# Kernel tuning notes

Measured on AMD Instinct MI355X. Metric: run time of the kernel, lower is better.

The kernel has to match this reference:

```python
import jax, jax.numpy as jnp
import numpy as np

EMBED_DIM = 2048
HEAD_DIM = 128
BLOCK = 2048
BATCH = 8


def setup_inputs() -> dict:
    key = jax.random.key(0)
    kx, kq, kk, kv = jax.random.split(key, 4)
    x = jax.random.normal(kx, (BATCH, BLOCK, EMBED_DIM), dtype=jnp.float32)
    # torch nn.Linear(embed_dim, head_dim, bias=False) weight shape: [head_dim, embed_dim]
    s = 1.0 / np.sqrt(EMBED_DIM)
    Wq = jax.random.uniform(kq, (HEAD_DIM, EMBED_DIM), jnp.float32, -s, s)
    Wk = jax.random.uniform(kk, (HEAD_DIM, EMBED_DIM), jnp.float32, -s, s)
    Wv = jax.random.uniform(kv, (HEAD_DIM, EMBED_DIM), jnp.float32, -s, s)
    return {"x": x, "Wq": Wq, "Wk": Wk, "Wv": Wv}


def reference(x, Wq, Wk, Wv):
    B, T, C = x.shape
    # projections: y = x @ W.T
    q = jnp.einsum('btc,hc->bth', x, Wq)   # [B,T,H]
    k = jnp.einsum('btc,hc->bth', x, Wk)
    v = jnp.einsum('btc,hc->bth', x, Wv)
    # NOTE: original scales by embed_dim**0.5, not head_dim**0.5
    scale = 1.0 / jnp.sqrt(jnp.float32(C))
    logits = jnp.einsum('bth,bsh->bts', q, k) * scale  # [B,T,T]
    # causal mask (is_decoder=True)
    causal = jnp.tril(jnp.ones((T, T), dtype=bool))
    logits = jnp.where(causal, logits, -jnp.inf)
    weights = jax.nn.softmax(logits, axis=-1)
    attention = jnp.einsum('bts,bsh->bth', weights, v)  # [B,T,H]
    return attention
```

## Files before the change

kernel.cpp:

```cpp
#include <hip/hip_runtime.h>
#include <hip/hip_bf16.h>
#include <stdint.h>

constexpr int B    = 8;
constexpr int T    = 2048;
constexpr int EMB  = 2048;
constexpr int HD   = 128;
constexpr int M    = B * T;
constexpr int NW   = 3 * HD;

typedef __attribute__((ext_vector_type(8))) short short8;
typedef __attribute__((ext_vector_type(4))) float f32x4;

__device__ inline unsigned short f2bf(float f) {
    union { float f; unsigned int u; } v; v.f = f;
    unsigned int x = v.u;
    unsigned int r = (x + 0x7FFFu + ((x >> 16) & 1u)) >> 16;
    return (unsigned short)r;
}

__device__ inline unsigned int cvt_pk_bf16(float a, float b) {
    unsigned int r;
    asm volatile("v_cvt_pk_bf16_f32 %0, %1, %2" : "=v"(r) : "v"(a), "v"(b));
    return r;
}

__global__ __launch_bounds__(256) void conv_w(
    const float* __restrict__ Wq, const float* __restrict__ Wk, const float* __restrict__ Wv,
    unsigned short* __restrict__ Wb)
{
    int base = (blockIdx.x * 256 + threadIdx.x) * 8;
    int row = base >> 11, col = base & 2047;
    const float* src;
    if (row < 128)      src = Wq + (size_t)row * EMB + col;
    else if (row < 256) src = Wk + (size_t)(row - 128) * EMB + col;
    else                src = Wv + (size_t)(row - 256) * EMB + col;
    float4 a = *(const float4*)src;
    float4 b = *(const float4*)(src + 4);
    short8 sv;
    sv[0] = f2bf(a.x); sv[1] = f2bf(a.y); sv[2] = f2bf(a.z); sv[3] = f2bf(a.w);
    sv[4] = f2bf(b.x); sv[5] = f2bf(b.y); sv[6] = f2bf(b.z); sv[7] = f2bf(b.w);
    *(short8*)(Wb + base) = sv;
}

constexpr int PBM = 64;
constexpr int PBK = 64;
constexpr int PNT = EMB / PBK;

__global__ __launch_bounds__(512) void qkv_proj(
    const float* __restrict__ x, const unsigned short* __restrict__ Wb,
    unsigned short* __restrict__ Qb, unsigned short* __restrict__ Kb,
    unsigned short* __restrict__ VtG)
{
    __shared__ unsigned short Asm[2][PBM * PBK];
    __shared__ unsigned short Bsm[2][NW * PBK];

    const int m0   = blockIdx.x * PBM;
    const int tid  = threadIdx.x;
    const int lane = tid & 63;
    const int w    = tid >> 6;
    const int wr   = w >> 2;
    const int wc   = w & 3;
    const int lo   = lane & 15;
    const int hi   = lane >> 4;

    const int ar = tid >> 3;
    const int as = tid & 7;
    const float* asrc = x + (size_t)(m0 + ar) * EMB + as * 8;

    f32x4 acc[2][6];
#pragma unroll
    for (int i = 0; i < 2; ++i)
#pragma unroll
        for (int j = 0; j < 6; ++j) acc[i][j] = (f32x4)0.0f;

    float4 a0, a1;
    auto issueA = [&](int k0) {
        a0 = *(const float4*)(asrc + k0);
        a1 = *(const float4*)(asrc + k0 + 4);
    };
    auto writeA = [&](int buf) {
        uint4 p;
        p.x = cvt_pk_bf16(a0.x, a0.y);
        p.y = cvt_pk_bf16(a0.z, a0.w);
        p.z = cvt_pk_bf16(a1.x, a1.y);
        p.w = cvt_pk_bf16(a1.z, a1.w);
        int ps = as ^ (ar & 7);
        *(uint4*)&Asm[buf][ar * PBK + ps * 8] = p;
    };
    auto stageB = [&](int k0, int buf) {
#pragma unroll
        for (int it = 0; it < 6; ++it) {
            int c = it * 512 + tid;
            int row = c >> 3;
            int lseg = (c & 7) ^ (row & 7);
            __builtin_amdgcn_global_load_lds(
                (const __attribute__((address_space(1))) unsigned int*)
                    (Wb + (size_t)row * EMB + k0 + lseg * 8),
                (__attribute__((address_space(3))) unsigned int*)
                    ((char*)&Bsm[buf][0] + (it * 512 + w * 64) * 16),
                16, 0, 0);
        }
    };
    auto compute = [&](int buf) {
#pragma unroll
        for (int kk = 0; kk < 2; ++kk) {
            short8 af[2], bf[6];
#pragma unroll
            for (int i = 0; i < 2; ++i) {
                int R = wr * 32 + i * 16 + lo;
                int pseg = (kk * 4 + hi) ^ (R & 7);
                af[i] = *(const short8*)&Asm[buf][R * PBK + pseg * 8];
            }
#pragma unroll
            for (int j = 0; j < 6; ++j) {
                int n = wc * 96 + j * 16 + lo;
                int pseg = (kk * 4 + hi) ^ (n & 7);
                bf[j] = *(const short8*)&Bsm[buf][n * PBK + pseg * 8];
            }
#pragma unroll
            for (int i = 0; i < 2; ++i)
#pragma unroll
                for (int j = 0; j < 6; ++j)
                    acc[i][j] = __builtin_amdgcn_mfma_f32_16x16x32_bf16(af[i], bf[j], acc[i][j], 0, 0, 0);
        }
    };

    issueA(0);
    stageB(0, 0);
    writeA(0);
    asm volatile("s_waitcnt vmcnt(0) lgkmcnt(0)" ::: "memory");
    __builtin_amdgcn_s_barrier();

    for (int t = 0; t < PNT; ++t) {
        const int buf = t & 1;
        if (t + 1 < PNT) {
            issueA((t + 1) * PBK);
            stageB((t + 1) * PBK, buf ^ 1);
        }
        compute(buf);
        if (t + 1 < PNT) {
            writeA(buf ^ 1);
            asm volatile("s_waitcnt vmcnt(0) lgkmcnt(0)" ::: "memory");
            __builtin_amdgcn_s_barrier();
        }
    }

    const int b = m0 >> 11;
#pragma unroll
    for (int i = 0; i < 2; ++i) {
        int mrow0 = m0 + wr * 32 + i * 16 + hi * 4;
#pragma unroll
        for (int j = 0; j < 6; ++j) {
            int cw = wc * 6 + j;
            int colbase = cw * 16 + lo;
            if (cw < 8) {
#pragma unroll
                for (int r = 0; r < 4; ++r)
                    Qb[(size_t)(mrow0 + r) * HD + colbase] = f2bf(acc[i][j][r]);
            } else if (cw < 16) {
#pragma unroll
                for (int r = 0; r < 4; ++r)
                    Kb[(size_t)(mrow0 + r) * HD + (colbase - 128)] = f2bf(acc[i][j][r]);
            } else {
                int h = colbase - 256;
                int tloc = mrow0 - b * T;
                ushort4 pv;
                pv.x = f2bf(acc[i][j][0]); pv.y = f2bf(acc[i][j][1]);
                pv.z = f2bf(acc[i][j][2]); pv.w = f2bf(acc[i][j][3]);
                *(ushort4*)(VtG + ((size_t)(b * HD + h)) * T + tloc) = pv;
            }
        }
    }
}

constexpr int QB = 64;
constexpr int KB = 64;
constexpr int STILES = 8;

__global__ __launch_bounds__(256) void attn_fwd(
    const unsigned short* __restrict__ Qb,
    const unsigned short* __restrict__ Kb,
    const unsigned short* __restrict__ VtG,
    float* __restrict__ out,
    float* __restrict__ part_o, float* __restrict__ part_ml,
    int use_split)
{
    const int b  = blockIdx.y;
    int bx = blockIdx.x;
    int qt, s, nsplit;
    if (use_split) {
        if (bx < 8)       { qt = bx;               s = 0; }
        else if (bx < 24) { qt = 8  + (bx - 8) / 2;  s = (bx - 8) & 1; }
        else if (bx < 48) { qt = 16 + (bx - 24) / 3; s = (bx - 24) % 3; }
        else              { qt = 24 + (bx - 48) / 4; s = (bx - 48) & 3; }
        nsplit = qt / 8 + 1;
    } else {
        qt = bx; s = 0; nsplit = 1;
    }
    const int q0 = qt * QB;
    int t0 = s * STILES;
    int t1 = t0 + STILES; if (t1 > qt + 1) t1 = qt + 1;

    const int tid  = threadIdx.x;
    const int lane = tid & 63;
    const int w    = tid >> 6;
    const int lo   = lane & 15;
    const int hi   = lane >> 4;

    __shared__ unsigned short Ks[KB][HD + 8];
    __shared__ unsigned short Vt[HD][KB + 16];
    __shared__ unsigned short Ps[QB][KB + 8];

    short8 qf[4];
    {
        int row = q0 + w * 16 + lo;
        const unsigned short* qp = Qb + ((size_t)b * T + row) * HD + hi * 8;
#pragma unroll
        for (int ks = 0; ks < 4; ++ks) qf[ks] = *(const short8*)(qp + ks * 32);
    }

    float mrow[4], lrow[4];
    f32x4 o[8];
#pragma unroll
    for (int r = 0; r < 4; ++r) { mrow[r] = -1e30f; lrow[r] = 0.0f; }
#pragma unroll
    for (int n = 0; n < 8; ++n) o[n] = (f32x4)0.0f;

    const float scale2 = 0.022097086912079608f * 1.4426950408889634f;
    const int qrow_base = q0 + w * 16 + hi * 4;

    for (int t = t0; t < t1; ++t) {
        const int kv0 = t * KB;
#pragma unroll
        for (int it = 0; it < 4; ++it) {
            int c = tid + it * 256;
            int row = c >> 4, c8 = (c & 15) * 8;
            *(short8*)&Ks[row][c8] =
                *(const short8*)(Kb + ((size_t)b * T + kv0 + row) * HD + c8);
        }
#pragma unroll
        for (int it = 0; it < 4; ++it) {
            int c = tid + it * 256;
            int row = c >> 3, c8 = (c & 7) * 8;
            *(short8*)&Vt[row][c8] =
                *(const short8*)(VtG + (size_t)(b * HD + row) * T + kv0 + c8);
        }
        __syncthreads();

        f32x4 sa[4];
#pragma unroll
        for (int j = 0; j < 4; ++j) sa[j] = (f32x4)0.0f;
#pragma unroll
        for (int ks = 0; ks < 4; ++ks) {
#pragma unroll
            for (int j = 0; j < 4; ++j) {
                short8 bf = *(const short8*)&Ks[j * 16 + lo][ks * 32 + hi * 8];
                sa[j] = __builtin_amdgcn_mfma_f32_16x16x32_bf16(qf[ks], bf, sa[j], 0, 0, 0);
            }
        }

        const bool diag = (t == qt);
        float alpha[4];
#pragma unroll
        for (int r = 0; r < 4; ++r) {
            const int qrow = qrow_base + r;
            float rm = -1e30f;
#pragma unroll
            for (int j = 0; j < 4; ++j) {
                float v = sa[j][r] * scale2;
                if (diag) {
                    int kv = kv0 + j * 16 + lo;
                    v = (kv <= qrow) ? v : -1e30f;
                }
                sa[j][r] = v;
                rm = fmaxf(rm, v);
            }
            rm = fmaxf(rm, __shfl_xor(rm, 1));
            rm = fmaxf(rm, __shfl_xor(rm, 2));
            rm = fmaxf(rm, __shfl_xor(rm, 4));
            rm = fmaxf(rm, __shfl_xor(rm, 8));
            float mn = fmaxf(mrow[r], rm);
            alpha[r] = exp2f(mrow[r] - mn);
            mrow[r] = mn;
            float ls = 0.0f;
#pragma unroll
            for (int j = 0; j < 4; ++j) {
                float p = exp2f(sa[j][r] - mn);
                sa[j][r] = p;
                ls += p;
            }
            ls += __shfl_xor(ls, 1);
            ls += __shfl_xor(ls, 2);
            ls += __shfl_xor(ls, 4);
            ls += __shfl_xor(ls, 8);
            lrow[r] = lrow[r] * alpha[r] + ls;
        }
#pragma unroll
        for (int n = 0; n < 8; ++n)
#pragma unroll
            for (int r = 0; r < 4; ++r) o[n][r] *= alpha[r];

#pragma unroll
        for (int r = 0; r < 4; ++r)
#pragma unroll
            for (int j = 0; j < 4; ++j)
                Ps[w * 16 + hi * 4 + r][j * 16 + lo] = f2bf(sa[j][r]);
        __syncthreads();

#pragma unroll
        for (int ks = 0; ks < 2; ++ks) {
            short8 af = *(const short8*)&Ps[w * 16 + lo][ks * 32 + hi * 8];
#pragma unroll
            for (int n = 0; n < 8; ++n) {
                short8 bv = *(const short8*)&Vt[n * 16 + lo][ks * 32 + hi * 8];
                o[n] = __builtin_amdgcn_mfma_f32_16x16x32_bf16(af, bv, o[n], 0, 0, 0);
            }
        }
        __syncthreads();
    }

    if (nsplit == 1) {
#pragma unroll
        for (int n = 0; n < 8; ++n) {
            int h = n * 16 + lo;
#pragma unroll
            for (int r = 0; r < 4; ++r) {
                int row = qrow_base + r;
                out[((size_t)b * T + row) * HD + h] = o[n][r] / lrow[r];
            }
        }
    } else {
        const size_t slot = (size_t)(b * 32 + qt) * 4 + s;
        float* po = part_o + slot * (QB * HD);
#pragma unroll
        for (int n = 0; n < 8; ++n) {
            int h = n * 16 + lo;
#pragma unroll
            for (int r = 0; r < 4; ++r)
                po[(w * 16 + hi * 4 + r) * HD + h] = o[n][r];
        }
        if (lo == 0) {
            float* pm = part_ml + slot * (QB * 2);
#pragma unroll
            for (int r = 0; r < 4; ++r) {
                pm[(w * 16 + hi * 4 + r) * 2 + 0] = mrow[r];
                pm[(w * 16 + hi * 4 + r) * 2 + 1] = lrow[r];
            }
        }
    }
}

__global__ __launch_bounds__(256) void attn_combine(
    const float* __restrict__ part_o, const float* __restrict__ part_ml,
    float* __restrict__ out)
{
    const int qt = 8 + blockIdx.x;
    const int b  = blockIdx.y;
    const int ns = qt / 8 + 1;
    const int tid = threadIdx.x;
    const int row = tid >> 2;
    const int c0  = (tid & 3) * 32;
    const size_t slot0 = (size_t)(b * 32 + qt) * 4;

    float mi[4], li[4];
    float m = -1e30f;
#pragma unroll 4
    for (int i = 0; i < ns; ++i) {
        mi[i] = part_ml[(slot0 + i) * (QB * 2) + row * 2 + 0];
        li[i] = part_ml[(slot0 + i) * (QB * 2) + row * 2 + 1];
        m = fmaxf(m, mi[i]);
    }
    float L = 0.0f, f[4];
#pragma unroll 4
    for (int i = 0; i < ns; ++i) {
        f[i] = exp2f(mi[i] - m);
        L += li[i] * f[i];
    }
    const float inv = 1.0f / L;

    float4 acc[8];
#pragma unroll
    for (int k = 0; k < 8; ++k) acc[k] = make_float4(0.f, 0.f, 0.f, 0.f);
#pragma unroll 4
    for (int i = 0; i < ns; ++i) {
        const float4* src = (const float4*)(part_o + (slot0 + i) * (QB * HD) + row * HD + c0);
#pragma unroll
        for (int k = 0; k < 8; ++k) {
            float4 v = src[k];
            acc[k].x += f[i] * v.x; acc[k].y += f[i] * v.y;
            acc[k].z += f[i] * v.z; acc[k].w += f[i] * v.w;
        }
    }
    float4* dst = (float4*)(out + ((size_t)b * T + qt * QB + row) * HD + c0);
#pragma unroll
    for (int k = 0; k < 8; ++k) {
        float4 v = acc[k];
        dst[k] = make_float4(v.x * inv, v.y * inv, v.z * inv, v.w * inv);
    }
}

extern "C" void kernel_launch(void* const* d_in, const int* in_sizes, int n_in,
                              void* d_out, int out_size, void* d_ws, size_t ws_size,
                              hipStream_t stream)
{
    const float* x  = (const float*)d_in[0];
    const float* Wq = (const float*)d_in[1];
    const float* Wk = (const float*)d_in[2];
    const float* Wv = (const float*)d_in[3];
    float* out = (float*)d_out;

    const size_t off_Wb = 0;
    const size_t off_Q  = off_Wb + (size_t)NW * EMB * 2;
    const size_t off_K  = off_Q  + (size_t)M * HD * 2;
    const size_t off_V  = off_K  + (size_t)M * HD * 2;
    const size_t off_po = off_V  + (size_t)M * HD * 2;
    const size_t off_ml = off_po + (size_t)1024 * QB * HD * 4;
    const size_t total  = off_ml + (size_t)1024 * QB * 2 * 4;

    char* ws = (char*)d_ws;
    unsigned short* Wb  = (unsigned short*)(ws + off_Wb);
    unsigned short* Qb  = (unsigned short*)(ws + off_Q);
    unsigned short* Kb  = (unsigned short*)(ws + off_K);
    unsigned short* VtG = (unsigned short*)(ws + off_V);
    float* part_o  = (float*)(ws + off_po);
    float* part_ml = (float*)(ws + off_ml);

    const int use_split = (ws_size >= total) ? 1 : 0;

    conv_w<<<dim3((NW * EMB) / (256 * 8)), 256, 0, stream>>>(Wq, Wk, Wv, Wb);
    qkv_proj<<<dim3(M / PBM), 512, 0, stream>>>(x, Wb, Qb, Kb, VtG);
    attn_fwd<<<dim3(use_split ? 80 : 32, B), 256, 0, stream>>>(
        Qb, Kb, VtG, out, part_o, part_ml, use_split);
    if (use_split)
        attn_combine<<<dim3(24, B), 256, 0, stream>>>(part_o, part_ml, out);
}
```

Before: 115.4 us.

## Deepen QKV projection pipeline to two tiles ahead and remap warps to columns

Restructures the QKV projection GEMM so loads for tile t+2 are issued while tile t is computed. Partial vmcnt waits keep the global loads in flight across the barrier instead of draining everything each step. It also changes the warp tiling from 2x4 to 1x8, so each warp covers all 64 rows and 48 columns. That raises A-fragment LDS reads per warp but lowers B reads. The hand-tuned waitcnt counts and sched_barriers add risk of hazards, and the manual unroll holds more live registers.

```diff
diff --git a/kernel.cpp b/kernel.cpp
--- a/kernel.cpp
+++ b/kernel.cpp
@@ -52,15 +52,13 @@
     unsigned short* __restrict__ Qb, unsigned short* __restrict__ Kb,
     unsigned short* __restrict__ VtG)
 {
-    __shared__ unsigned short Asm[2][PBM * PBK];
-    __shared__ unsigned short Bsm[2][NW * PBK];
+    __shared__ unsigned short Ab[2][PBM * PBK];
+    __shared__ unsigned short Bb[2][NW * PBK];
 
     const int m0   = blockIdx.x * PBM;
     const int tid  = threadIdx.x;
     const int lane = tid & 63;
     const int w    = tid >> 6;
-    const int wr   = w >> 2;
-    const int wc   = w & 3;
     const int lo   = lane & 15;
     const int hi   = lane >> 4;
 
@@ -68,26 +66,12 @@
     const int as = tid & 7;
     const float* asrc = x + (size_t)(m0 + ar) * EMB + as * 8;
 
-    f32x4 acc[2][6];
-#pragma unroll
-    for (int i = 0; i < 2; ++i)
-#pragma unroll
-        for (int j = 0; j < 6; ++j) acc[i][j] = (f32x4)0.0f;
-
-    float4 a0, a1;
-    auto issueA = [&](int k0) {
-        a0 = *(const float4*)(asrc + k0);
-        a1 = *(const float4*)(asrc + k0 + 4);
-    };
-    auto writeA = [&](int buf) {
-        uint4 p;
-        p.x = cvt_pk_bf16(a0.x, a0.y);
-        p.y = cvt_pk_bf16(a0.z, a0.w);
-        p.z = cvt_pk_bf16(a1.x, a1.y);
-        p.w = cvt_pk_bf16(a1.z, a1.w);
-        int ps = as ^ (ar & 7);
-        *(uint4*)&Asm[buf][ar * PBK + ps * 8] = p;
-    };
+    f32x4 acc[4][3];
+#pragma unroll
+    for (int i = 0; i < 4; ++i)
+#pragma unroll
+        for (int j = 0; j < 3; ++j) acc[i][j] = (f32x4)0.0f;
+
     auto stageB = [&](int k0, int buf) {
 #pragma unroll
         for (int it = 0; it < 6; ++it) {
@@ -98,61 +82,108 @@
                 (const __attribute__((address_space(1))) unsigned int*)
                     (Wb + (size_t)row * EMB + k0 + lseg * 8),
                 (__attribute__((address_space(3))) unsigned int*)
-                    ((char*)&Bsm[buf][0] + (it * 512 + w * 64) * 16),
+                    ((char*)&Bb[buf][0] + (it * 512 + w * 64) * 16),
                 16, 0, 0);
         }
+    };
+    auto writeA = [&](int buf, float4 A0, float4 A1) {
+        uint4 p;
+        p.x = cvt_pk_bf16(A0.x, A0.y);
+        p.y = cvt_pk_bf16(A0.z, A0.w);
+        p.z = cvt_pk_bf16(A1.x, A1.y);
+        p.w = cvt_pk_bf16(A1.z, A1.w);
+        int ps = as ^ (ar & 7);
+        *(uint4*)&Ab[buf][ar * PBK + ps * 8] = p;
     };
     auto compute = [&](int buf) {
 #pragma unroll
         for (int kk = 0; kk < 2; ++kk) {
-            short8 af[2], bf[6];
-#pragma unroll
-            for (int i = 0; i < 2; ++i) {
-                int R = wr * 32 + i * 16 + lo;
-                int pseg = (kk * 4 + hi) ^ (R & 7);
-                af[i] = *(const short8*)&Asm[buf][R * PBK + pseg * 8];
-            }
-#pragma unroll
-            for (int j = 0; j < 6; ++j) {
-                int n = wc * 96 + j * 16 + lo;
-                int pseg = (kk * 4 + hi) ^ (n & 7);
-                bf[j] = *(const short8*)&Bsm[buf][n * PBK + pseg * 8];
-            }
-#pragma unroll
-            for (int i = 0; i < 2; ++i)
-#pragma unroll
-                for (int j = 0; j < 6; ++j)
+            short8 af[4], bf[3];
+            const int cseg = kk * 4 + hi;
+#pragma unroll
+            for (int i = 0; i < 4; ++i) {
+                int R = i * 16 + lo;
+                af[i] = *(const short8*)&Ab[buf][R * PBK + (cseg ^ (R & 7)) * 8];
+            }
+#pragma unroll
+            for (int j = 0; j < 3; ++j) {
+                int n = w * 48 + j * 16 + lo;
+                bf[j] = *(const short8*)&Bb[buf][n * PBK + (cseg ^ (n & 7)) * 8];
+            }
+#pragma unroll
+            for (int i = 0; i < 4; ++i)
+#pragma unroll
+                for (int j = 0; j < 3; ++j)
                     acc[i][j] = __builtin_amdgcn_mfma_f32_16x16x32_bf16(af[i], bf[j], acc[i][j], 0, 0, 0);
         }
     };
 
-    issueA(0);
+    float4 a0e, a1e, a0o, a1o;
+
+    a0e = *(const float4*)(asrc + 0);
+    a1e = *(const float4*)(asrc + 4);
+    __builtin_amdgcn_sched_barrier(0);
     stageB(0, 0);
-    writeA(0);
-    asm volatile("s_waitcnt vmcnt(0) lgkmcnt(0)" ::: "memory");
+    __builtin_amdgcn_sched_barrier(0);
+    a0o = *(const float4*)(asrc + PBK);
+    a1o = *(const float4*)(asrc + PBK + 4);
+    __builtin_amdgcn_sched_barrier(0);
+    stageB(PBK, 1);
+    __builtin_amdgcn_sched_barrier(0);
+    asm volatile("s_waitcnt vmcnt(8)" ::: "memory");
+    __builtin_amdgcn_sched_barrier(0);
+    writeA(0, a0e, a1e);
+    asm volatile("s_waitcnt lgkmcnt(0)" ::: "memory");
+    __builtin_amdgcn_sched_barrier(0);
     __builtin_amdgcn_s_barrier();
 
-    for (int t = 0; t < PNT; ++t) {
-        const int buf = t & 1;
-        if (t + 1 < PNT) {
-            issueA((t + 1) * PBK);
-            stageB((t + 1) * PBK, buf ^ 1);
-        }
-        compute(buf);
-        if (t + 1 < PNT) {
-            writeA(buf ^ 1);
-            asm volatile("s_waitcnt vmcnt(0) lgkmcnt(0)" ::: "memory");
-            __builtin_amdgcn_s_barrier();
-        }
+#pragma unroll 1
+    for (int tt = 0; tt < PNT / 2; ++tt) {
+        const int t = tt * 2;
+        compute(0);
+        __builtin_amdgcn_s_barrier();
+        if (t + 2 < PNT) {
+            a0e = *(const float4*)(asrc + (t + 2) * PBK);
+            a1e = *(const float4*)(asrc + (t + 2) * PBK + 4);
+            __builtin_amdgcn_sched_barrier(0);
+            stageB((t + 2) * PBK, 0);
+            __builtin_amdgcn_sched_barrier(0);
+            asm volatile("s_waitcnt vmcnt(8)" ::: "memory");
+        } else {
+            asm volatile("s_waitcnt vmcnt(0)" ::: "memory");
+        }
+        __builtin_amdgcn_sched_barrier(0);
+        writeA(1, a0o, a1o);
+        asm volatile("s_waitcnt lgkmcnt(0)" ::: "memory");
+        __builtin_amdgcn_sched_barrier(0);
+        __builtin_amdgcn_s_barrier();
+        compute(1);
+        if (t + 1 == PNT - 1) break;
+        __builtin_amdgcn_s_barrier();
+        if (t + 3 < PNT) {
+            a0o = *(const float4*)(asrc + (t + 3) * PBK);
+            a1o = *(const float4*)(asrc + (t + 3) * PBK + 4);
+            __builtin_amdgcn_sched_barrier(0);
+            stageB((t + 3) * PBK, 1);
+            __builtin_amdgcn_sched_barrier(0);
+            asm volatile("s_waitcnt vmcnt(8)" ::: "memory");
+        } else {
+            asm volatile("s_waitcnt vmcnt(0)" ::: "memory");
+        }
+        __builtin_amdgcn_sched_barrier(0);
+        writeA(0, a0e, a1e);
+        asm volatile("s_waitcnt lgkmcnt(0)" ::: "memory");
+        __builtin_amdgcn_sched_barrier(0);
+        __builtin_amdgcn_s_barrier();
     }
 
     const int b = m0 >> 11;
 #pragma unroll
-    for (int i = 0; i < 2; ++i) {
-        int mrow0 = m0 + wr * 32 + i * 16 + hi * 4;
-#pragma unroll
-        for (int j = 0; j < 6; ++j) {
-            int cw = wc * 6 + j;
+    for (int i = 0; i < 4; ++i) {
+        int mrow0 = m0 + i * 16 + hi * 4;
+#pragma unroll
+        for (int j = 0; j < 3; ++j) {
+            int cw = w * 3 + j;
             int colbase = cw * 16 + lo;
             if (cw < 8) {
 #pragma unroll
```

Result: faster. 111.9 us (-3.0%).

## Stage QKV weight tiles through registers and re-split warps across N

Applied to the files above, without the earlier changes.

Replaces the direct global-to-LDS async loads for the weight tile with register-staged loads that are then written to swizzled LDS, matching how the activation tile is handled. Changes the per-wave tiling from a 2x4 warp grid (32 rows x 96 cols) to each of the 8 waves covering all 64 rows and 48 columns, with sched_barriers to keep the loads ahead of the MFMAs. This shifts how many LDS fragment reads each wave issues per MFMA and adds register pressure for the staged B data.

```diff
diff --git a/kernel.cpp b/kernel.cpp
--- a/kernel.cpp
+++ b/kernel.cpp
@@ -52,15 +52,13 @@
     unsigned short* __restrict__ Qb, unsigned short* __restrict__ Kb,
     unsigned short* __restrict__ VtG)
 {
-    __shared__ unsigned short Asm[2][PBM * PBK];
-    __shared__ unsigned short Bsm[2][NW * PBK];
+    __shared__ unsigned short Ab[2][PBM * PBK];
+    __shared__ unsigned short Bb[2][NW * PBK];
 
     const int m0   = blockIdx.x * PBM;
     const int tid  = threadIdx.x;
     const int lane = tid & 63;
     const int w    = tid >> 6;
-    const int wr   = w >> 2;
-    const int wc   = w & 3;
     const int lo   = lane & 15;
     const int hi   = lane >> 4;
 
@@ -68,91 +66,88 @@
     const int as = tid & 7;
     const float* asrc = x + (size_t)(m0 + ar) * EMB + as * 8;
 
-    f32x4 acc[2][6];
-#pragma unroll
-    for (int i = 0; i < 2; ++i)
-#pragma unroll
-        for (int j = 0; j < 6; ++j) acc[i][j] = (f32x4)0.0f;
-
+    f32x4 acc[4][3];
+#pragma unroll
+    for (int i = 0; i < 4; ++i)
+#pragma unroll
+        for (int j = 0; j < 3; ++j) acc[i][j] = (f32x4)0.0f;
+
+    short8 breg[6];
     float4 a0, a1;
-    auto issueA = [&](int k0) {
+
+    auto loadTile = [&](int k0) {
+#pragma unroll
+        for (int it = 0; it < 6; ++it) {
+            int c = it * 512 + tid;
+            int row = c >> 3, seg = c & 7;
+            breg[it] = *(const short8*)(Wb + (size_t)row * EMB + k0 + seg * 8);
+        }
         a0 = *(const float4*)(asrc + k0);
         a1 = *(const float4*)(asrc + k0 + 4);
     };
-    auto writeA = [&](int buf) {
+    auto writeTile = [&](int buf) {
+#pragma unroll
+        for (int it = 0; it < 6; ++it) {
+            int c = it * 512 + tid;
+            int row = c >> 3, seg = c & 7;
+            *(short8*)&Bb[buf][row * PBK + ((seg ^ (row & 7))) * 8] = breg[it];
+        }
         uint4 p;
         p.x = cvt_pk_bf16(a0.x, a0.y);
         p.y = cvt_pk_bf16(a0.z, a0.w);
         p.z = cvt_pk_bf16(a1.x, a1.y);
         p.w = cvt_pk_bf16(a1.z, a1.w);
-        int ps = as ^ (ar & 7);
-        *(uint4*)&Asm[buf][ar * PBK + ps * 8] = p;
-    };
-    auto stageB = [&](int k0, int buf) {
-#pragma unroll
-        for (int it = 0; it < 6; ++it) {
-            int c = it * 512 + tid;
-            int row = c >> 3;
-            int lseg = (c & 7) ^ (row & 7);
-            __builtin_amdgcn_global_load_lds(
-                (const __attribute__((address_space(1))) unsigned int*)
-                    (Wb + (size_t)row * EMB + k0 + lseg * 8),
-                (__attribute__((address_space(3))) unsigned int*)
-                    ((char*)&Bsm[buf][0] + (it * 512 + w * 64) * 16),
-                16, 0, 0);
-        }
+        *(uint4*)&Ab[buf][ar * PBK + (as ^ (ar & 7)) * 8] = p;
     };
     auto compute = [&](int buf) {
 #pragma unroll
         for (int kk = 0; kk < 2; ++kk) {
-            short8 af[2], bf[6];
-#pragma unroll
-            for (int i = 0; i < 2; ++i) {
-                int R = wr * 32 + i * 16 + lo;
-                int pseg = (kk * 4 + hi) ^ (R & 7);
-                af[i] = *(const short8*)&Asm[buf][R * PBK + pseg * 8];
-            }
-#pragma unroll
-            for (int j = 0; j < 6; ++j) {
-                int n = wc * 96 + j * 16 + lo;
-                int pseg = (kk * 4 + hi) ^ (n & 7);
-                bf[j] = *(const short8*)&Bsm[buf][n * PBK + pseg * 8];
-            }
-#pragma unroll
-            for (int i = 0; i < 2; ++i)
-#pragma unroll
-                for (int j = 0; j < 6; ++j)
+            short8 af[4], bf[3];
+            const int cseg = kk * 4 + hi;
+#pragma unroll
+            for (int i = 0; i < 4; ++i) {
+                int R = i * 16 + lo;
+                af[i] = *(const short8*)&Ab[buf][R * PBK + (cseg ^ (R & 7)) * 8];
+            }
+#pragma unroll
+            for (int j = 0; j < 3; ++j) {
+                int n = w * 48 + j * 16 + lo;
+                bf[j] = *(const short8*)&Bb[buf][n * PBK + (cseg ^ (n & 7)) * 8];
+            }
+#pragma unroll
+            for (int i = 0; i < 4; ++i)
+#pragma unroll
+                for (int j = 0; j < 3; ++j)
                     acc[i][j] = __builtin_amdgcn_mfma_f32_16x16x32_bf16(af[i], bf[j], acc[i][j], 0, 0, 0);
         }
     };
 
-    issueA(0);
-    stageB(0, 0);
-    writeA(0);
-    asm volatile("s_waitcnt vmcnt(0) lgkmcnt(0)" ::: "memory");
-    __builtin_amdgcn_s_barrier();
-
+    loadTile(0);
+    writeTile(0);
+    __syncthreads();
+
+#pragma unroll 1
     for (int t = 0; t < PNT; ++t) {
         const int buf = t & 1;
         if (t + 1 < PNT) {
-            issueA((t + 1) * PBK);
-            stageB((t + 1) * PBK, buf ^ 1);
+            loadTile((t + 1) * PBK);
+            __builtin_amdgcn_sched_barrier(0);
         }
         compute(buf);
         if (t + 1 < PNT) {
-            writeA(buf ^ 1);
-            asm volatile("s_waitcnt vmcnt(0) lgkmcnt(0)" ::: "memory");
-            __builtin_amdgcn_s_barrier();
+            __builtin_amdgcn_sched_barrier(0);
+            writeTile(buf ^ 1);
+            __syncthreads();
         }
     }
 
     const int b = m0 >> 11;
 #pragma unroll
-    for (int i = 0; i < 2; ++i) {
-        int mrow0 = m0 + wr * 32 + i * 16 + hi * 4;
-#pragma unroll
-        for (int j = 0; j < 6; ++j) {
-            int cw = wc * 6 + j;
+    for (int i = 0; i < 4; ++i) {
+        int mrow0 = m0 + i * 16 + hi * 4;
+#pragma unroll
+        for (int j = 0; j < 3; ++j) {
+            int cw = w * 3 + j;
             int colbase = cw * 16 + lo;
             if (cw < 8) {
 #pragma unroll
```

Measured after the change: 102.6 us. 11.1% less time.
